# Optimization experiments

Hardware: AMD Instinct MI355X
Metric: run time of the kernel (lower is better)

The kernel has to match this reference:

```python
import jax, jax.numpy as jnp
import numpy as np

N_NODES = 50000
N_EDGES = 800000
IN_DIM = 89
HID = 128


def gcn_conv(x, src, dst, deg_inv_sqrt, W, b):
    # PyG GCNConv: x' = D^{-1/2} (A + I) D^{-1/2} (x W) + b
    h = x @ W  # [N, F_out]
    norm = deg_inv_sqrt[src] * deg_inv_sqrt[dst]  # per-edge norm [E]
    msgs = h[src] * norm[:, None]  # gather + scale [E, F_out]
    agg = jax.ops.segment_sum(msgs, dst, num_segments=x.shape[0])
    # self-loop contribution: norm = deg_inv_sqrt[i]^2
    agg = agg + h * (deg_inv_sqrt * deg_inv_sqrt)[:, None]
    return agg + b


def setup_inputs() -> dict:
    key = jax.random.key(0)
    k1, k2, k3, k4, k5, k6 = jax.random.split(key, 6)
    x = jax.random.normal(k1, (N_NODES, IN_DIM), dtype=jnp.float32)
    edge_index = jax.random.randint(k2, (2, N_EDGES), 0, N_NODES, dtype=jnp.int64)
    # Glorot-style init for GCN weights
    W1 = jax.random.normal(k3, (IN_DIM, HID), dtype=jnp.float32) * (1.0 / np.sqrt(IN_DIM))
    b1 = jnp.zeros((HID,), dtype=jnp.float32)
    W2 = jax.random.normal(k4, (HID, HID), dtype=jnp.float32) * (1.0 / np.sqrt(HID))
    b2 = jnp.zeros((HID,), dtype=jnp.float32)
    return {"x": x, "edge_index": edge_index, "W1": W1, "b1": b1, "W2": W2, "b2": b2}


def reference(x, edge_index, W1, b1, W2, b2):
    src = edge_index[0]
    dst = edge_index[1]
    n = x.shape[0]
    # degree of A + I: 1 (self loop) + in-degree
    deg = 1.0 + jax.ops.segment_sum(jnp.ones((src.shape[0],), x.dtype), dst, num_segments=n)
    deg_inv_sqrt = jax.lax.rsqrt(deg)
    h = jax.nn.relu(gcn_conv(x, src, dst, deg_inv_sqrt, W1, b1))
    h = jax.nn.relu(gcn_conv(h, src, dst, deg_inv_sqrt, W2, b2))
    return (h, edge_index)
```

## Files before the change

kernel.cpp:

```cpp
#include <hip/hip_runtime.h>
#include <hip/hip_bf16.h>


#define HID 128
#define KIN 89
#define KP 96
#define BSH 7
#define BNODES 128
#define MAXBUCK 512
#define NPB 128
#define P4CAP 3072

typedef __attribute__((ext_vector_type(8))) short bf16x8;
typedef __attribute__((ext_vector_type(4))) float f32x4;

static __device__ inline float2 unpack_bf16(unsigned v) {
    union { unsigned u; float f; } lo, hi;
    lo.u = v << 16;
    hi.u = v & 0xFFFF0000u;
    return make_float2(lo.f, hi.f);
}

static __device__ inline unsigned pack_bf16(float a, float b) {
    __hip_bfloat162 h = __float22bfloat162_rn(make_float2(a, b));
    return *reinterpret_cast<unsigned*>(&h);
}

static __device__ inline unsigned short f2bf(float v) {
    __hip_bfloat16 h = __float2bfloat16(v);
    return *reinterpret_cast<unsigned short*>(&h);
}

__global__ __launch_bounds__(256) void p1_kernel(
    const int* __restrict__ ei, float* __restrict__ outE,
    int* __restrict__ histG,
    const float* __restrict__ W1, unsigned short* __restrict__ W1t,
    const float* __restrict__ W2, unsigned short* __restrict__ W2t,
    int E, int nbuck)
{
    __shared__ int h[MAXBUCK];
    const int tid = threadIdx.x, blk = blockIdx.x;
    const int* src = ei;
    const int* dst = ei + E;
    for (int b = tid; b < nbuck; b += 256) h[b] = 0;

    int tg = blk * 256 + tid;
    if (tg < HID * KP) {
        int n = tg / KP, k = tg % KP;
        W1t[tg] = f2bf(k < KIN ? W1[(size_t)k * HID + n] : 0.0f);
    } else {
        int t2 = tg - HID * KP;
        if (t2 < HID * HID) {
            int n = t2 / HID, k = t2 % HID;
            W2t[t2] = f2bf(W2[(size_t)k * HID + n]);
        }
    }
    __syncthreads();

    const int chunk = (E + NPB - 1) / NPB;
    const int beg = blk * chunk, end = min(beg + chunk, E);
    for (int i = beg + tid; i < end; i += 256) {
        int d = dst[i];
        atomicAdd(&h[d >> BSH], 1);
        outE[i] = (float)src[i];
        outE[E + i] = (float)d;
    }
    __syncthreads();
    for (int b = tid; b < nbuck; b += 256) histG[b * NPB + blk] = h[b];
}

__global__ __launch_bounds__(NPB) void p2a_kernel(
    int* __restrict__ histG, int* __restrict__ totals)
{
    __shared__ int wsum[NPB / 64];
    const int b = blockIdx.x, tid = threadIdx.x, lane = tid & 63, wid = tid >> 6;
    int c = histG[b * NPB + tid];
    int s = c;
#pragma unroll
    for (int off = 1; off < 64; off <<= 1) {
        int t = __shfl_up(s, off, 64);
        if (lane >= off) s += t;
    }
    if (lane == 63) wsum[wid] = s;
    __syncthreads();
    if (tid == 0) {
        int a = 0;
#pragma unroll
        for (int w = 0; w < NPB / 64; ++w) { int t = wsum[w]; wsum[w] = a; a += t; }
    }
    __syncthreads();
    int excl = wsum[wid] + s - c;
    histG[b * NPB + tid] = excl;
    if (tid == NPB - 1) totals[b] = excl + c;
}

static __device__ inline void scan_totals2(const int* __restrict__ totals,
                                           int* __restrict__ sexcl,
                                           int* __restrict__ wsum,
                                           int nbuck, int tid)
{
    const int lane = tid & 63, wid = tid >> 6;
    const int i0 = 2 * tid, i1 = 2 * tid + 1;
    int t0 = (i0 < nbuck) ? totals[i0] : 0;
    int t1 = (i1 < nbuck) ? totals[i1] : 0;
    int p = t0 + t1;
    int s = p;
#pragma unroll
    for (int off = 1; off < 64; off <<= 1) {
        int t = __shfl_up(s, off, 64);
        if (lane >= off) s += t;
    }
    if (lane == 63) wsum[wid] = s;
    __syncthreads();
    if (tid == 0) {
        int a = 0;
#pragma unroll
        for (int w = 0; w < 4; ++w) { int t = wsum[w]; wsum[w] = a; a += t; }
    }
    __syncthreads();
    int excl = wsum[wid] + s - p;
    sexcl[i0] = excl;
    sexcl[i1] = excl + t0;
}

__global__ __launch_bounds__(256) void p3_part_kernel(
    const int* __restrict__ ei, const int* __restrict__ histG,
    const int* __restrict__ totals, unsigned* __restrict__ ebuf,
    int E, int nbuck)
{
    __shared__ int cur[MAXBUCK];
    __shared__ int wsum[4];
    const int tid = threadIdx.x, blk = blockIdx.x;
    const int* src = ei;
    const int* dst = ei + E;
    scan_totals2(totals, cur, wsum, nbuck, tid);
    __syncthreads();
    for (int b = tid; b < nbuck; b += 256) cur[b] += histG[b * NPB + blk];
    const int chunk = (E + NPB - 1) / NPB;
    const int beg = blk * chunk, end = min(beg + chunk, E);
    __syncthreads();
    for (int i = beg + tid; i < end; i += 256) {
        int d = dst[i];
        int b = d >> BSH;
        int pos = atomicAdd(&cur[b], 1);
        ebuf[pos] = ((unsigned)(d & (BNODES - 1)) << 16) | (unsigned)src[i];
    }
}

__global__ __launch_bounds__(256) void p4_sort_kernel(
    const unsigned* __restrict__ ebuf, const int* __restrict__ totals,
    unsigned short* __restrict__ csr, int* __restrict__ rowptr,
    float* __restrict__ dis, int N, int E, int nbuck)
{
    __shared__ int counts[BNODES];
    __shared__ int cursor[BNODES];
    __shared__ int sbase[MAXBUCK];
    __shared__ int wsum[4];
    __shared__ int w2[2];
    __shared__ unsigned short staging[P4CAP];
    const int b = blockIdx.x, tid = threadIdx.x, lane = tid & 63, wid = tid >> 6;

    scan_totals2(totals, sbase, wsum, nbuck, tid);
    __syncthreads();
    const int gbase = sbase[b];
    const int cnt = totals[b];

    if (tid < BNODES) counts[tid] = 0;
    __syncthreads();
    for (int i = tid; i < cnt; i += 256)
        atomicAdd(&counts[ebuf[gbase + i] >> 16], 1);
    __syncthreads();

    int c = 0, s = 0;
    if (tid < BNODES) {
        c = counts[tid];
        s = c;
#pragma unroll
        for (int off = 1; off < 64; off <<= 1) {
            int t = __shfl_up(s, off, 64);
            if (lane >= off) s += t;
        }
        if (lane == 63) w2[wid] = s;
    }
    __syncthreads();
    if (tid == 0) { int t = w2[0]; w2[0] = 0; w2[1] = t; }
    __syncthreads();
    if (tid < BNODES) {
        int excl = w2[wid] + s - c;
        cursor[tid] = excl;
        int node = b * BNODES + tid;
        if (node < N) {
            rowptr[node] = gbase + excl;
            dis[node] = rsqrtf(1.0f + (float)c);
        }
    }
    if (b == 0 && tid == 0) rowptr[N] = E;
    __syncthreads();

    if (cnt <= P4CAP) {
        for (int i = tid; i < cnt; i += 256) {
            unsigned v = ebuf[gbase + i];
            int pos = atomicAdd(&cursor[v >> 16], 1);
            staging[pos] = (unsigned short)(v & 0xFFFFu);
        }
        __syncthreads();
        for (int i = tid; i < cnt; i += 256)
            csr[gbase + i] = staging[i];
    } else {
        for (int i = tid; i < cnt; i += 256) {
            unsigned v = ebuf[gbase + i];
            int pos = atomicAdd(&cursor[v >> 16], 1);
            csr[gbase + pos] = (unsigned short)(v & 0xFFFFu);
        }
    }
}

__global__ __launch_bounds__(256) void xconv_kernel(
    const float* __restrict__ X, const float* __restrict__ dis,
    unsigned* __restrict__ Xhs, int N)
{
    int t = blockIdx.x * 256 + threadIdx.x;
    if (t >= N * (KP / 2)) return;
    int n = t / (KP / 2), c = t % (KP / 2);
    float d = dis[n];
    const float* xr = X + (size_t)n * KIN;
    float a = (2 * c     < KIN) ? d * xr[2 * c]     : 0.0f;
    float b = (2 * c + 1 < KIN) ? d * xr[2 * c + 1] : 0.0f;
    Xhs[t] = pack_bf16(a, b);
}

__global__ __launch_bounds__(256) void gather_x_kernel(
    const unsigned* __restrict__ rows, const int* __restrict__ rowptr,
    const unsigned short* __restrict__ csr, unsigned* __restrict__ aggh, int N)
{
    int node = blockIdx.x * 4 + (threadIdx.x >> 6);
    if (node >= N) return;
    int lane = threadIdx.x & 63;
    bool act = lane < (KP / 2);

    float a0 = 0.0f, a1 = 0.0f;
    if (act) {
        float2 v = unpack_bf16(rows[(size_t)node * (KP / 2) + lane]);
        a0 = v.x; a1 = v.y;
    }

    int beg = rowptr[node], end = rowptr[node + 1];
    int j = beg;
    for (; j + 4 <= end; j += 4) {
        int s0 = csr[j], s1 = csr[j + 1], s2 = csr[j + 2], s3 = csr[j + 3];
        if (act) {
            float2 v0 = unpack_bf16(rows[(size_t)s0 * (KP / 2) + lane]);
            float2 v1 = unpack_bf16(rows[(size_t)s1 * (KP / 2) + lane]);
            float2 v2 = unpack_bf16(rows[(size_t)s2 * (KP / 2) + lane]);
            float2 v3 = unpack_bf16(rows[(size_t)s3 * (KP / 2) + lane]);
            a0 += v0.x + v1.x + v2.x + v3.x;
            a1 += v0.y + v1.y + v2.y + v3.y;
        }
    }
    for (; j < end; ++j) {
        int sx = csr[j];
        if (act) {
            float2 v = unpack_bf16(rows[(size_t)sx * (KP / 2) + lane]);
            a0 += v.x; a1 += v.y;
        }
    }
    if (act)
        aggh[(size_t)node * (KP / 2) + lane] = pack_bf16(a0, a1);
}

__global__ __launch_bounds__(256) void gather_h_kernel(
    const unsigned* __restrict__ rows, const int* __restrict__ rowptr,
    const unsigned short* __restrict__ csr, unsigned* __restrict__ aggh, int N)
{
    int node = blockIdx.x * 4 + (threadIdx.x >> 6);
    if (node >= N) return;
    int lane = threadIdx.x & 63;
    int beg = rowptr[node], end = rowptr[node + 1];

    float2 sv = unpack_bf16(rows[(size_t)node * (HID / 2) + lane]);
    float a0 = sv.x, a1 = sv.y;
    int j = beg;
    for (; j + 4 <= end; j += 4) {
        int s0 = csr[j], s1 = csr[j + 1], s2 = csr[j + 2], s3 = csr[j + 3];
        float2 v0 = unpack_bf16(rows[(size_t)s0 * (HID / 2) + lane]);
        float2 v1 = unpack_bf16(rows[(size_t)s1 * (HID / 2) + lane]);
        float2 v2 = unpack_bf16(rows[(size_t)s2 * (HID / 2) + lane]);
        float2 v3 = unpack_bf16(rows[(size_t)s3 * (HID / 2) + lane]);
        a0 += v0.x + v1.x + v2.x + v3.x;
        a1 += v0.y + v1.y + v2.y + v3.y;
    }
    for (; j < end; ++j) {
        int sx = csr[j];
        float2 v = unpack_bf16(rows[(size_t)sx * (HID / 2) + lane]);
        a0 += v.x; a1 += v.y;
    }
    aggh[(size_t)node * (HID / 2) + lane] = pack_bf16(a0, a1);
}

template<int KPA, bool LAYER1>
__global__ __launch_bounds__(256) void mfma_gemm_kernel(
    const unsigned short* __restrict__ A, const unsigned short* __restrict__ Wt,
    const float* __restrict__ bias, const float* __restrict__ dis,
    void* __restrict__ outp, int N)
{
    const int wave = threadIdx.x >> 6;
    const int lane = threadIdx.x & 63;
    const int m    = lane & 15;
    const int quad = lane >> 4;
    const int row0 = blockIdx.x * 64 + wave * 16;
    const int node = row0 + m;

    f32x4 acc[8];
#pragma unroll
    for (int t = 0; t < 8; ++t) acc[t] = (f32x4){0.0f, 0.0f, 0.0f, 0.0f};

    const int arow = min(node, N - 1);
    const unsigned short* arp = A + (size_t)arow * KPA;

#pragma unroll
    for (int c = 0; c < KPA / 32; ++c) {
        const int k0 = c * 32 + quad * 8;
        bf16x8 nv = *(const bf16x8*)(arp + k0);
#pragma unroll
        for (int t = 0; t < 8; ++t) {
            bf16x8 wv = *(const bf16x8*)(Wt + (size_t)(t * 16 + m) * KPA + k0);
            acc[t] = __builtin_amdgcn_mfma_f32_16x16x32_bf16(wv, nv, acc[t], 0, 0, 0);
        }
    }

    if (node < N) {
        const float dv = dis[node];
#pragma unroll
        for (int t = 0; t < 8; ++t) {
            const int col0 = t * 16 + quad * 4;
            float4 bb = *(const float4*)&bias[col0];
            float r0 = fmaxf(fmaf(dv, acc[t][0], bb.x), 0.0f);
            float r1 = fmaxf(fmaf(dv, acc[t][1], bb.y), 0.0f);
            float r2 = fmaxf(fmaf(dv, acc[t][2], bb.z), 0.0f);
            float r3 = fmaxf(fmaf(dv, acc[t][3], bb.w), 0.0f);
            if (LAYER1) {
                uint2 u;
                u.x = pack_bf16(r0 * dv, r1 * dv);
                u.y = pack_bf16(r2 * dv, r3 * dv);
                *(uint2*)((unsigned short*)outp + (size_t)node * HID + col0) = u;
            } else {
                float4 r = make_float4(r0, r1, r2, r3);
                *(float4*)((float*)outp + (size_t)node * HID + col0) = r;
            }
        }
    }
}


static inline char* wsal(char*& p, size_t n) {
    uintptr_t q = ((uintptr_t)p + 255) & ~(uintptr_t)255;
    char* r = (char*)q;
    p = r + n;
    return r;
}

extern "C" void kernel_launch(void* const* d_in, const int* in_sizes, int n_in,
                              void* d_out, int out_size, void* d_ws, size_t ws_size,
                              hipStream_t stream) {
    const float* x  = (const float*)d_in[0];
    const int*   ei = (const int*)d_in[1];
    const float* W1 = (const float*)d_in[2];
    const float* b1 = (const float*)d_in[3];
    const float* W2 = (const float*)d_in[4];
    const float* b2 = (const float*)d_in[5];

    const int N = in_sizes[0] / KIN;
    const int E = in_sizes[1] / 2;
    const int nbuck = (N + BNODES - 1) >> BSH;

    float* out  = (float*)d_out;
    float* outH = out;
    float* outE = out + (size_t)N * HID;

    char* ws = (char*)d_ws;
    int*            histG  = (int*)wsal(ws, (size_t)MAXBUCK * NPB * 4);
    int*            totals = (int*)wsal(ws, MAXBUCK * 4);
    int*            rowptr = (int*)wsal(ws, (size_t)(N + 1) * 4);
    float*          dis    = (float*)wsal(ws, (size_t)N * 4);
    unsigned*       ebuf   = (unsigned*)wsal(ws, (size_t)E * 4);
    unsigned short* csr    = (unsigned short*)wsal(ws, (size_t)E * 2);
    unsigned*       Xhs    = (unsigned*)wsal(ws, (size_t)N * (KP / 2) * 4);
    unsigned*       agg1h  = (unsigned*)wsal(ws, (size_t)N * (KP / 2) * 4);
    unsigned short* g2h    = (unsigned short*)wsal(ws, (size_t)N * HID * 2);
    unsigned short* agg2h  = (unsigned short*)wsal(ws, (size_t)N * HID * 2);
    unsigned short* W1t    = (unsigned short*)wsal(ws, (size_t)HID * KP * 2);
    unsigned short* W2t    = (unsigned short*)wsal(ws, (size_t)HID * HID * 2);

    p1_kernel<<<NPB, 256, 0, stream>>>(ei, outE, histG, W1, W1t, W2, W2t, E, nbuck);
    p2a_kernel<<<nbuck, NPB, 0, stream>>>(histG, totals);
    p3_part_kernel<<<NPB, 256, 0, stream>>>(ei, histG, totals, ebuf, E, nbuck);
    p4_sort_kernel<<<nbuck, 256, 0, stream>>>(ebuf, totals, csr, rowptr, dis,
                                              N, E, nbuck);
    xconv_kernel<<<(N * (KP / 2) + 255) / 256, 256, 0, stream>>>(x, dis, Xhs, N);

    const int ngt = (N + 3) / 4;
    const int ngm = (N + 63) / 64;

    gather_x_kernel<<<ngt, 256, 0, stream>>>(Xhs, rowptr, csr, agg1h, N);
    mfma_gemm_kernel<KP, true><<<ngm, 256, 0, stream>>>(
        (const unsigned short*)agg1h, W1t, b1, dis, g2h, N);

    gather_h_kernel<<<ngt, 256, 0, stream>>>((const unsigned*)g2h, rowptr, csr,
                                             (unsigned*)agg2h, N);
    mfma_gemm_kernel<HID, false><<<ngm, 256, 0, stream>>>(
        agg2h, W2t, b2, dis, outH, N);
}
```

Baseline: 232.8 us.

## Unify gather kernels with half-wave edge split and 8-byte vector loads

Replaces the two per-layer gather kernels with one kernel in which each half-wave handles alternate edges and each lane loads 8 bytes (4 bf16), then the halves are combined with a cross-half shuffle. This doubles the number of edges in flight per wave and widens each load, aiming to improve memory-level parallelism in the latency-bound neighbor gather. To share the kernel, the layer-1 input padding grows from 96 to 128 columns, which adds about a third more bytes per row to the layer-1 gather and xconv and more K work to the layer-1 GEMM.

```diff
diff --git a/kernel.cpp b/kernel.cpp
--- a/kernel.cpp
+++ b/kernel.cpp
@@ -4,7 +4,7 @@
 
 #define HID 128
 #define KIN 89
-#define KP 96
+#define KP 128
 #define BSH 7
 #define BNODES 128
 #define MAXBUCK 512
@@ -229,72 +229,72 @@
     Xhs[t] = pack_bf16(a, b);
 }
 
-__global__ __launch_bounds__(256) void gather_x_kernel(
-    const unsigned* __restrict__ rows, const int* __restrict__ rowptr,
-    const unsigned short* __restrict__ csr, unsigned* __restrict__ aggh, int N)
+__global__ __launch_bounds__(256) void gather_kernel(
+    const uint2* __restrict__ rows, const int* __restrict__ rowptr,
+    const unsigned short* __restrict__ csr, uint2* __restrict__ aggh, int N)
 {
     int node = blockIdx.x * 4 + (threadIdx.x >> 6);
     if (node >= N) return;
-    int lane = threadIdx.x & 63;
-    bool act = lane < (KP / 2);
-
-    float a0 = 0.0f, a1 = 0.0f;
-    if (act) {
-        float2 v = unpack_bf16(rows[(size_t)node * (KP / 2) + lane]);
-        a0 = v.x; a1 = v.y;
-    }
-
-    int beg = rowptr[node], end = rowptr[node + 1];
+    const int lane = threadIdx.x & 63;
+    const int half = lane >> 5;
+    const int sl   = lane & 31;
+
+    float a0 = 0.0f, a1 = 0.0f, a2 = 0.0f, a3 = 0.0f;
+    if (half == 0) {
+        uint2 sv = rows[(size_t)node * 32 + sl];
+        float2 lo = unpack_bf16(sv.x), hi = unpack_bf16(sv.y);
+        a0 = lo.x; a1 = lo.y; a2 = hi.x; a3 = hi.y;
+    }
+
+    const int beg = rowptr[node], end = rowptr[node + 1];
     int j = beg;
+    for (; j + 8 <= end; j += 8) {
+        int r0 = csr[j     + half];
+        int r1 = csr[j + 2 + half];
+        int r2 = csr[j + 4 + half];
+        int r3 = csr[j + 6 + half];
+        uint2 v0 = rows[(size_t)r0 * 32 + sl];
+        uint2 v1 = rows[(size_t)r1 * 32 + sl];
+        uint2 v2 = rows[(size_t)r2 * 32 + sl];
+        uint2 v3 = rows[(size_t)r3 * 32 + sl];
+        float2 p;
+        p = unpack_bf16(v0.x); a0 += p.x; a1 += p.y;
+        p = unpack_bf16(v0.y); a2 += p.x; a3 += p.y;
+        p = unpack_bf16(v1.x); a0 += p.x; a1 += p.y;
+        p = unpack_bf16(v1.y); a2 += p.x; a3 += p.y;
+        p = unpack_bf16(v2.x); a0 += p.x; a1 += p.y;
+        p = unpack_bf16(v2.y); a2 += p.x; a3 += p.y;
+        p = unpack_bf16(v3.x); a0 += p.x; a1 += p.y;
+        p = unpack_bf16(v3.y); a2 += p.x; a3 += p.y;
+    }
     for (; j + 4 <= end; j += 4) {
-        int s0 = csr[j], s1 = csr[j + 1], s2 = csr[j + 2], s3 = csr[j + 3];
-        if (act) {
-            float2 v0 = unpack_bf16(rows[(size_t)s0 * (KP / 2) + lane]);
-            float2 v1 = unpack_bf16(rows[(size_t)s1 * (KP / 2) + lane]);
-            float2 v2 = unpack_bf16(rows[(size_t)s2 * (KP / 2) + lane]);
-            float2 v3 = unpack_bf16(rows[(size_t)s3 * (KP / 2) + lane]);
-            a0 += v0.x + v1.x + v2.x + v3.x;
-            a1 += v0.y + v1.y + v2.y + v3.y;
-        }
-    }
-    for (; j < end; ++j) {
-        int sx = csr[j];
-        if (act) {
-            float2 v = unpack_bf16(rows[(size_t)sx * (KP / 2) + lane]);
-            a0 += v.x; a1 += v.y;
-        }
-    }
-    if (act)
-        aggh[(size_t)node * (KP / 2) + lane] = pack_bf16(a0, a1);
-}
-
-__global__ __launch_bounds__(256) void gather_h_kernel(
-    const unsigned* __restrict__ rows, const int* __restrict__ rowptr,
-    const unsigned short* __restrict__ csr, unsigned* __restrict__ aggh, int N)
-{
-    int node = blockIdx.x * 4 + (threadIdx.x >> 6);
-    if (node >= N) return;
-    int lane = threadIdx.x & 63;
-    int beg = rowptr[node], end = rowptr[node + 1];
-
-    float2 sv = unpack_bf16(rows[(size_t)node * (HID / 2) + lane]);
-    float a0 = sv.x, a1 = sv.y;
-    int j = beg;
-    for (; j + 4 <= end; j += 4) {
-        int s0 = csr[j], s1 = csr[j + 1], s2 = csr[j + 2], s3 = csr[j + 3];
-        float2 v0 = unpack_bf16(rows[(size_t)s0 * (HID / 2) + lane]);
-        float2 v1 = unpack_bf16(rows[(size_t)s1 * (HID / 2) + lane]);
-        float2 v2 = unpack_bf16(rows[(size_t)s2 * (HID / 2) + lane]);
-        float2 v3 = unpack_bf16(rows[(size_t)s3 * (HID / 2) + lane]);
-        a0 += v0.x + v1.x + v2.x + v3.x;
-        a1 += v0.y + v1.y + v2.y + v3.y;
-    }
-    for (; j < end; ++j) {
-        int sx = csr[j];
-        float2 v = unpack_bf16(rows[(size_t)sx * (HID / 2) + lane]);
-        a0 += v.x; a1 += v.y;
-    }
-    aggh[(size_t)node * (HID / 2) + lane] = pack_bf16(a0, a1);
+        int r0 = csr[j     + half];
+        int r1 = csr[j + 2 + half];
+        uint2 v0 = rows[(size_t)r0 * 32 + sl];
+        uint2 v1 = rows[(size_t)r1 * 32 + sl];
+        float2 p;
+        p = unpack_bf16(v0.x); a0 += p.x; a1 += p.y;
+        p = unpack_bf16(v0.y); a2 += p.x; a3 += p.y;
+        p = unpack_bf16(v1.x); a0 += p.x; a1 += p.y;
+        p = unpack_bf16(v1.y); a2 += p.x; a3 += p.y;
+    }
+    for (; j < end; j += 2) {
+        int idx = j + half;
+        if (idx < end) {
+            int r = csr[idx];
+            uint2 v = rows[(size_t)r * 32 + sl];
+            float2 lo = unpack_bf16(v.x), hi = unpack_bf16(v.y);
+            a0 += lo.x; a1 += lo.y; a2 += hi.x; a3 += hi.y;
+        }
+    }
+
+    a0 += __shfl_xor(a0, 32, 64);
+    a1 += __shfl_xor(a1, 32, 64);
+    a2 += __shfl_xor(a2, 32, 64);
+    a3 += __shfl_xor(a3, 32, 64);
+    if (half == 0)
+        aggh[(size_t)node * 32 + sl] =
+            make_uint2(pack_bf16(a0, a1), pack_bf16(a2, a3));
 }
 
 template<int KPA, bool LAYER1>
@@ -401,12 +401,13 @@
     const int ngt = (N + 3) / 4;
     const int ngm = (N + 63) / 64;
 
-    gather_x_kernel<<<ngt, 256, 0, stream>>>(Xhs, rowptr, csr, agg1h, N);
+    gather_kernel<<<ngt, 256, 0, stream>>>((const uint2*)Xhs, rowptr, csr,
+                                           (uint2*)agg1h, N);
     mfma_gemm_kernel<KP, true><<<ngm, 256, 0, stream>>>(
         (const unsigned short*)agg1h, W1t, b1, dis, g2h, N);
 
-    gather_h_kernel<<<ngt, 256, 0, stream>>>((const unsigned*)g2h, rowptr, csr,
-                                             (unsigned*)agg2h, N);
+    gather_kernel<<<ngt, 256, 0, stream>>>((const uint2*)g2h, rowptr, csr,
+                                           (uint2*)agg2h, N);
     mfma_gemm_kernel<HID, false><<<ngm, 256, 0, stream>>>(
         agg2h, W2t, b2, dis, outH, N);
 }
```

Measured after the change: 232.3 us. About the same (-0.2%).
